# Performance work log

Measured on AMD Instinct MI355X. Metric: run time of the kernel, lower is better.

The kernel has to match this reference:

```python
import jax, jax.numpy as jnp
import numpy as np
from jax import lax

B, S, H, L, NH, DH, FF, C, V, P = 8, 512, 768, 12, 12, 64, 3072, 9, 30522, 512
INV_SQRT_DH = 1.0 / float(np.sqrt(DH))

def _ln(x, s, b, eps=1e-12):
    m = x.mean(-1, keepdims=True)
    v = x.var(-1, keepdims=True)
    return (x - m) / jnp.sqrt(v + eps) * s + b

def _encode(input_ids, attention_mask, fl):
    (tok_emb, pos_emb, type_emb, emb_ln_s, emb_ln_b, qkv_w, qkv_b, ao_w, ao_b,
     ln1_s, ln1_b, ff1_w, ff1_b, ff2_w, ff2_b, ln2_s, ln2_b, head_w, head_b,
     trans, start_t, end_t) = fl
    x = tok_emb[input_ids] + pos_emb[None, :S] + type_emb[0]   # token_type_ids=None -> all zeros
    x = _ln(x, emb_ln_s, emb_ln_b)
    bias = (1.0 - attention_mask.astype(x.dtype))[:, None, None, :] * -1e4
    for i in range(L):
        qkv = x @ qkv_w[i] + qkv_b[i]
        q, k, v = [t.reshape(B, S, NH, DH).transpose(0, 2, 1, 3) for t in jnp.split(qkv, 3, axis=-1)]
        a = jax.nn.softmax(jnp.einsum('bhqd,bhkd->bhqk', q, k) * INV_SQRT_DH + bias, axis=-1)
        ctx = jnp.einsum('bhqk,bhkd->bhqd', a, v).transpose(0, 2, 1, 3).reshape(B, S, H)
        x = _ln(x + ctx @ ao_w[i] + ao_b[i], ln1_s[i], ln1_b[i])
        hmid = jax.nn.gelu(x @ ff1_w[i] + ff1_b[i], approximate=False)
        x = _ln(x + hmid @ ff2_w[i] + ff2_b[i], ln2_s[i], ln2_b[i])
    return x @ head_w + head_b  # emissions [B,S,C]; dropout is identity in eval

def _crf_llh(em, tags, mask, trans, start_t, end_t):
    # pytorch-crf: sum over batch of (numerator - log partition)
    b = jnp.arange(em.shape[0])
    mf = mask.astype(em.dtype)
    num = start_t[tags[:, 0]] + em[b, 0, tags[:, 0]]
    tr = trans[tags[:, :-1], tags[:, 1:]]                                    # [B,S-1]
    es = jnp.take_along_axis(em[:, 1:], tags[:, 1:, None], axis=2)[..., 0]   # [B,S-1]
    num = num + jnp.sum((tr + es) * mf[:, 1:], axis=1)
    last = (mask.sum(1) - 1).astype(jnp.int32)
    num = num + end_t[jnp.take_along_axis(tags, last[:, None], 1)[:, 0]]
    def step(alpha, xs):
        e_t, m_t = xs  # [B,C], [B]
        nxt = jax.scipy.special.logsumexp(alpha[:, :, None] + trans[None] + e_t[:, None, :], axis=1)
        return jnp.where(m_t[:, None], nxt, alpha), None
    alpha0 = start_t + em[:, 0]
    alpha, _ = lax.scan(step, alpha0, (em[:, 1:].transpose(1, 0, 2), mask[:, 1:].T))
    logZ = jax.scipy.special.logsumexp(alpha + end_t, axis=1)
    return jnp.sum(num - logZ)

def _viterbi(em, mask, trans, start_t, end_t):
    def step(score, xs):
        e_t, m_t = xs
        cand = score[:, :, None] + trans[None]   # [B,C,C]
        idx = jnp.argmax(cand, axis=1)           # [B,C] backpointers
        best = jnp.max(cand, axis=1) + e_t
        return jnp.where(m_t[:, None], best, score), idx
    score, hist = lax.scan(step, start_t + em[:, 0], (em[:, 1:].transpose(1, 0, 2), mask[:, 1:].T))
    last = jnp.argmax(score + end_t, axis=1)     # [B]
    def back(tag, xs):
        idx_t, m_t = xs
        prev = jnp.take_along_axis(idx_t, tag[:, None], 1)[:, 0]
        return jnp.where(m_t, prev, tag), tag
    first, rest = lax.scan(back, last, (hist, mask[:, 1:].T), reverse=True)
    return jnp.concatenate([first[:, None], rest.T], axis=1)  # [B,S]

def setup_inputs():
    key = jax.random.key(0)
    ks = iter(jax.random.split(key, 32))
    p = lambda shape, s=0.02: (jax.random.normal(next(ks), shape) * s).astype(jnp.float32)
    return dict(
        input_ids=jax.random.randint(next(ks), (B, S), 0, V),
        attention_mask=jnp.ones((B, S), dtype=jnp.int32),
        labels=jax.random.randint(next(ks), (B, S), 0, C),
        tok_emb=p((V, H)), pos_emb=p((P, H)), type_emb=p((2, H)),
        emb_ln_s=jnp.ones((H,), jnp.float32), emb_ln_b=jnp.zeros((H,), jnp.float32),
        qkv_w=p((L, H, 3 * H)), qkv_b=jnp.zeros((L, 3 * H), jnp.float32),
        ao_w=p((L, H, H)), ao_b=jnp.zeros((L, H), jnp.float32),
        ln1_s=jnp.ones((L, H), jnp.float32), ln1_b=jnp.zeros((L, H), jnp.float32),
        ff1_w=p((L, H, FF)), ff1_b=jnp.zeros((L, FF), jnp.float32),
        ff2_w=p((L, FF, H)), ff2_b=jnp.zeros((L, H), jnp.float32),
        ln2_s=jnp.ones((L, H), jnp.float32), ln2_b=jnp.zeros((L, H), jnp.float32),
        head_w=p((H, C)), head_b=jnp.zeros((C,), jnp.float32),
        trans=p((C, C), 0.1), start_t=p((C,), 0.1), end_t=p((C,), 0.1),
    )

def reference(input_ids, attention_mask, labels, tok_emb, pos_emb, type_emb, emb_ln_s, emb_ln_b,
              qkv_w, qkv_b, ao_w, ao_b, ln1_s, ln1_b, ff1_w, ff1_b, ff2_w, ff2_b, ln2_s, ln2_b,
              head_w, head_b, trans, start_t, end_t):
    fl = (tok_emb, pos_emb, type_emb, emb_ln_s, emb_ln_b, qkv_w, qkv_b, ao_w, ao_b,
          ln1_s, ln1_b, ff1_w, ff1_b, ff2_w, ff2_b, ln2_s, ln2_b, head_w, head_b,
          trans, start_t, end_t)
    em = _encode(input_ids, attention_mask, fl)
    mask = attention_mask.astype(bool)
    neg_llh = -_crf_llh(em, labels, mask, trans, start_t, end_t)
    tags = _viterbi(em, mask, trans, start_t, end_t)
    return (neg_llh, tags)
```

## Files before the change

### kernel.cpp

```cpp
#include <hip/hip_runtime.h>
#include <hip/hip_bf16.h>
#include <math.h>

#define HDIM 768
#define SEQ 512
#define BATCH 8
#define NHEAD 12
#define DHEAD 64
#define FFDIM 3072
#define NLAYER 12
#define NCLS 9

typedef _Float16 half8 __attribute__((ext_vector_type(8)));
typedef _Float16 half4v __attribute__((ext_vector_type(4)));
typedef float f32x4 __attribute__((ext_vector_type(4)));

#define OFF_QKV 0
#define OFF_AO  (768*2304)
#define OFF_FF1 (768*2304 + 768*768)
#define OFF_FF2 (768*2304 + 768*768 + 768*3072)
#define WELEMS  (768*2304 + 768*768 + 768*3072 + 3072*768)

__device__ __forceinline__ float block_sum_256(float v, float* red) {
  #pragma unroll
  for (int o = 32; o > 0; o >>= 1) v += __shfl_down(v, o);
  int t = threadIdx.x;
  if ((t & 63) == 0) red[t >> 6] = v;
  __syncthreads();
  float r = red[0] + red[1] + red[2] + red[3];
  __syncthreads();
  return r;
}

__global__ __launch_bounds__(256) void embed_ln_kernel(
    const int* __restrict__ ids, const float* __restrict__ tok,
    const float* __restrict__ pos, const float* __restrict__ typ,
    const float* __restrict__ gamma, const float* __restrict__ beta,
    float* __restrict__ xout)
{
  __shared__ float red[4];
  int row = blockIdx.x;
  int t = threadIdx.x;
  int s = row & (SEQ - 1);
  int id = ids[row];
  float v[3];
  #pragma unroll
  for (int k = 0; k < 3; k++) {
    int d = t + k * 256;
    v[k] = tok[(size_t)id * HDIM + d] + pos[(size_t)s * HDIM + d] + typ[d];
  }
  float total = block_sum_256(v[0] + v[1] + v[2], red);
  float mean = total * (1.0f / 768.0f);
  float sq = 0.0f;
  #pragma unroll
  for (int k = 0; k < 3; k++) { float d = v[k] - mean; sq += d * d; }
  float var = block_sum_256(sq, red) * (1.0f / 768.0f);
  float inv = rsqrtf(var + 1e-12f);
  #pragma unroll
  for (int k = 0; k < 3; k++) {
    int d = t + k * 256;
    xout[(size_t)row * HDIM + d] = (v[k] - mean) * inv * gamma[d] + beta[d];
  }
}

__global__ __launch_bounds__(256) void ln_kernel(
    const float* __restrict__ in, const float* __restrict__ gamma,
    const float* __restrict__ beta, float* __restrict__ outp)
{
  __shared__ float red[4];
  int row = blockIdx.x, t = threadIdx.x;
  const float* ip = in + (size_t)row * HDIM;
  float v[3];
  #pragma unroll
  for (int k = 0; k < 3; k++) v[k] = ip[t + k * 256];
  float total = block_sum_256(v[0] + v[1] + v[2], red);
  float mean = total * (1.0f / 768.0f);
  float sq = 0.0f;
  #pragma unroll
  for (int k = 0; k < 3; k++) { float d = v[k] - mean; sq += d * d; }
  float var = block_sum_256(sq, red) * (1.0f / 768.0f);
  float inv = rsqrtf(var + 1e-12f);
  float* op = outp + (size_t)row * HDIM;
  #pragma unroll
  for (int k = 0; k < 3; k++) {
    int d = t + k * 256;
    op[d] = (v[k] - mean) * inv * gamma[d] + beta[d];
  }
}

__global__ __launch_bounds__(256) void convert_w_kernel(
    const float* __restrict__ w_qkv, const float* __restrict__ w_ao,
    const float* __restrict__ w_ff1, const float* __restrict__ w_ff2,
    _Float16* __restrict__ hi, _Float16* __restrict__ lo)
{
  int bid = blockIdx.x;
  const float* src; int K, N; size_t off; int tb;
  if (bid < 432)       { src = w_qkv; K = 768;  N = 2304; off = OFF_QKV; tb = bid; }
  else if (bid < 576)  { src = w_ao;  K = 768;  N = 768;  off = OFF_AO;  tb = bid - 432; }
  else if (bid < 1152) { src = w_ff1; K = 768;  N = 3072; off = OFF_FF1; tb = bid - 576; }
  else                 { src = w_ff2; K = 3072; N = 768;  off = OFF_FF2; tb = bid - 1152; }
  int ntn = N >> 6;
  int k0 = (tb / ntn) * 64, n0 = (tb % ntn) * 64;
  __shared__ float tile[64][65];
  int t = threadIdx.x;
  int r = t >> 4, c4 = (t & 15) * 4;
  #pragma unroll
  for (int i = 0; i < 4; i++) {
    float4 v = *(const float4*)(src + (size_t)(k0 + r + 16 * i) * N + n0 + c4);
    tile[r + 16 * i][c4 + 0] = v.x;
    tile[r + 16 * i][c4 + 1] = v.y;
    tile[r + 16 * i][c4 + 2] = v.z;
    tile[r + 16 * i][c4 + 3] = v.w;
  }
  __syncthreads();
  #pragma unroll
  for (int o = 0; o < 4; o++) {
    int n = r + 16 * o;
    half4v hv, lv;
    #pragma unroll
    for (int j = 0; j < 4; j++) {
      float x = tile[c4 + j][n];
      _Float16 h = (_Float16)x;
      hv[j] = h;
      lv[j] = (_Float16)(x - (float)h);
    }
    size_t idx = off + (size_t)(n0 + n) * K + k0 + c4;
    *(half4v*)&hi[idx] = hv;
    *(half4v*)&lo[idx] = lv;
  }
}

__device__ __forceinline__ float gelu_exact(float x) {
  return 0.5f * x * (1.0f + erff(x * 0.70710678118654752440f));
}

template<int BM, bool GELU, bool RES>
__global__ __launch_bounds__(256) void gemm_mfma(
    const float* __restrict__ A, const _Float16* __restrict__ WTh,
    const _Float16* __restrict__ WTl, const float* __restrict__ bias,
    const float* __restrict__ Rsrc, float* __restrict__ C,
    int M, int N, int K)
{
  constexpr int MI = BM / 32;
  constexpr int TPR = 256 / BM;
  constexpr int AW = BM / 8;
  __shared__ _Float16 Ah[BM][40], Al[BM][40];
  __shared__ _Float16 Bh[128][40], Bl[128][40];

  int t = threadIdx.x;
  int n0 = blockIdx.x * 128, m0 = blockIdx.y * BM;
  int wave = t >> 6, lane = t & 63;
  int wm = (wave >> 1) * (BM / 2), wn = (wave & 1) * 64;
  int r15 = lane & 15, kg = lane >> 4;

  int ar = t / TPR, ac = (t % TPR) * AW;
  int br = t >> 1, bc = (t & 1) * 16;
  const float* Ap = A + (size_t)(m0 + ar) * K + ac;
  const _Float16* Bph = WTh + (size_t)(n0 + br) * K + bc;
  const _Float16* Bpl = WTl + (size_t)(n0 + br) * K + bc;

  f32x4 acc[MI][4];
  #pragma unroll
  for (int i = 0; i < MI; i++)
    #pragma unroll
    for (int j = 0; j < 4; j++) acc[i][j] = (f32x4){0.f, 0.f, 0.f, 0.f};

  for (int k0 = 0; k0 < K; k0 += 32) {
    float af[AW];
    #pragma unroll
    for (int c = 0; c < AW / 4; c++) {
      float4 v = *(const float4*)(Ap + k0 + c * 4);
      af[c * 4 + 0] = v.x; af[c * 4 + 1] = v.y;
      af[c * 4 + 2] = v.z; af[c * 4 + 3] = v.w;
    }
    float4 bh0 = *(const float4*)(Bph + k0);
    float4 bh1 = *(const float4*)(Bph + k0 + 8);
    float4 bl0 = *(const float4*)(Bpl + k0);
    float4 bl1 = *(const float4*)(Bpl + k0 + 8);

    __syncthreads();
    #pragma unroll
    for (int c = 0; c < AW / 8; c++) {
      half8 hv, lv;
      #pragma unroll
      for (int e = 0; e < 8; e++) {
        float x = af[c * 8 + e];
        _Float16 h = (_Float16)x;
        hv[e] = h;
        lv[e] = (_Float16)(x - (float)h);
      }
      *(half8*)&Ah[ar][ac + c * 8] = hv;
      *(half8*)&Al[ar][ac + c * 8] = lv;
    }
    *(float4*)&Bh[br][bc]     = bh0;
    *(float4*)&Bh[br][bc + 8] = bh1;
    *(float4*)&Bl[br][bc]     = bl0;
    *(float4*)&Bl[br][bc + 8] = bl1;
    __syncthreads();

    half8 ahf[MI], alf[MI];
    #pragma unroll
    for (int i = 0; i < MI; i++) {
      ahf[i] = *(const half8*)&Ah[wm + i * 16 + r15][kg * 8];
      alf[i] = *(const half8*)&Al[wm + i * 16 + r15][kg * 8];
    }
    #pragma unroll
    for (int j = 0; j < 4; j++) {
      half8 bhf = *(const half8*)&Bh[wn + j * 16 + r15][kg * 8];
      half8 blf = *(const half8*)&Bl[wn + j * 16 + r15][kg * 8];
      #pragma unroll
      for (int i = 0; i < MI; i++) {
        acc[i][j] = __builtin_amdgcn_mfma_f32_16x16x32_f16(ahf[i], bhf, acc[i][j], 0, 0, 0);
        acc[i][j] = __builtin_amdgcn_mfma_f32_16x16x32_f16(ahf[i], blf, acc[i][j], 0, 0, 0);
        acc[i][j] = __builtin_amdgcn_mfma_f32_16x16x32_f16(alf[i], bhf, acc[i][j], 0, 0, 0);
      }
    }
  }

  #pragma unroll
  for (int i = 0; i < MI; i++)
    #pragma unroll
    for (int j = 0; j < 4; j++)
      #pragma unroll
      for (int q = 0; q < 4; q++) {
        int row = m0 + wm + i * 16 + kg * 4 + q;
        int col = n0 + wn + j * 16 + r15;
        float v = acc[i][j][q] + bias[col];
        if (RES) v += Rsrc[(size_t)row * N + col];
        if (GELU) v = gelu_exact(v);
        C[(size_t)row * N + col] = v;
      }
}

__device__ __forceinline__ int swz(int jl, int d) {
  return jl * 64 + ((((d) >> 3) ^ (jl & 7)) << 3) + ((d) & 7);
}

__global__ __launch_bounds__(256) void attn_kernel(
    const float* __restrict__ qkv, const int* __restrict__ maskp,
    float* __restrict__ ctxo)
{
  __shared__ float ss[16][516];
  __shared__ float qs[16][68];
  __shared__ float ks[64 * 64];

  int t = threadIdx.x;
  int qt = blockIdx.x, bh = blockIdx.y;
  int b = bh / NHEAD, h = bh % NHEAD;
  int q0 = qt * 16;
  const float* Qb = qkv + (size_t)b * SEQ * 2304 + h * 64;
  const float* Kb = Qb + 768;
  const float* Vb = Qb + 1536;

  {
    int r = t >> 4, d0 = (t & 15) * 4;
    *(float4*)&qs[r][d0] = *(const float4*)(Qb + (size_t)(q0 + r) * 2304 + d0);
  }
  __syncthreads();

  int r = t >> 4, j16 = t & 15;

  for (int jt = 0; jt < 8; jt++) {
    int kr = t >> 2, kc0 = (t & 3) * 16;
    const float* src = Kb + (size_t)(jt * 64 + kr) * 2304 + kc0;
    float4 kv0 = *(const float4*)(src + 0);
    float4 kv1 = *(const float4*)(src + 4);
    float4 kv2 = *(const float4*)(src + 8);
    float4 kv3 = *(const float4*)(src + 12);
    __syncthreads();
    *(float4*)&ks[swz(kr, kc0 + 0)]  = kv0;
    *(float4*)&ks[swz(kr, kc0 + 4)]  = kv1;
    *(float4*)&ks[swz(kr, kc0 + 8)]  = kv2;
    *(float4*)&ks[swz(kr, kc0 + 12)] = kv3;
    __syncthreads();
    float sacc[4] = {0, 0, 0, 0};
    #pragma unroll
    for (int d0 = 0; d0 < 64; d0 += 4) {
      float4 qv = *(const float4*)&qs[r][d0];
      #pragma unroll
      for (int jj = 0; jj < 4; jj++) {
        int jl = jj * 16 + j16;
        float4 kv = *(const float4*)&ks[swz(jl, d0)];
        sacc[jj] += qv.x * kv.x + qv.y * kv.y + qv.z * kv.z + qv.w * kv.w;
      }
    }
    #pragma unroll
    for (int jj = 0; jj < 4; jj++) {
      int j = jt * 64 + jj * 16 + j16;
      float mb = (1.0f - (float)maskp[b * SEQ + j]) * -10000.0f;
      ss[r][j] = sacc[jj] * 0.125f + mb;
    }
    __syncthreads();
  }

  {
    float mx = -1e30f;
    for (int j = j16; j < 512; j += 16) mx = fmaxf(mx, ss[r][j]);
    #pragma unroll
    for (int o = 1; o < 16; o <<= 1) mx = fmaxf(mx, __shfl_xor(mx, o));
    float l = 0.0f;
    for (int j = j16; j < 512; j += 16) {
      float p = expf(ss[r][j] - mx);
      ss[r][j] = p;
      l += p;
    }
    #pragma unroll
    for (int o = 1; o < 16; o <<= 1) l += __shfl_xor(l, o);
    float inv = 1.0f / l;
    for (int j = j16; j < 512; j += 16) ss[r][j] *= inv;
  }
  __syncthreads();

  int dl = t & 15;
  float acc[4] = {0, 0, 0, 0};
  for (int jt = 0; jt < 8; jt++) {
    int kr = t >> 2, kc0 = (t & 3) * 16;
    const float* src = Vb + (size_t)(jt * 64 + kr) * 2304 + kc0;
    float4 kv0 = *(const float4*)(src + 0);
    float4 kv1 = *(const float4*)(src + 4);
    float4 kv2 = *(const float4*)(src + 8);
    float4 kv3 = *(const float4*)(src + 12);
    __syncthreads();
    *(float4*)&ks[swz(kr, kc0 + 0)]  = kv0;
    *(float4*)&ks[swz(kr, kc0 + 4)]  = kv1;
    *(float4*)&ks[swz(kr, kc0 + 8)]  = kv2;
    *(float4*)&ks[swz(kr, kc0 + 12)] = kv3;
    __syncthreads();
    #pragma unroll
    for (int jl4 = 0; jl4 < 16; jl4++) {
      float4 pv = *(const float4*)&ss[r][jt * 64 + jl4 * 4];
      float pl[4] = {pv.x, pv.y, pv.z, pv.w};
      #pragma unroll
      for (int q = 0; q < 4; q++) {
        int jl = jl4 * 4 + q;
        float4 kv = *(const float4*)&ks[swz(jl, dl * 4)];
        acc[0] += pl[q] * kv.x;
        acc[1] += pl[q] * kv.y;
        acc[2] += pl[q] * kv.z;
        acc[3] += pl[q] * kv.w;
      }
    }
    __syncthreads();
  }
  float4 outv = {acc[0], acc[1], acc[2], acc[3]};
  *(float4*)(ctxo + (size_t)(b * SEQ + q0 + r) * HDIM + h * 64 + dl * 4) = outv;
}

__global__ __launch_bounds__(256) void head_kernel(
    const float* __restrict__ x, const float* __restrict__ W,
    const float* __restrict__ bias, float* __restrict__ em)
{
  int wid = threadIdx.x >> 6, lane = threadIdx.x & 63;
  int row = blockIdx.x * 4 + wid;
  const float* xp = x + (size_t)row * HDIM;
  float xv[12];
  #pragma unroll
  for (int k = 0; k < 12; k++) xv[k] = xp[lane + k * 64];
  for (int c = 0; c < NCLS; c++) {
    float p = 0.0f;
    #pragma unroll
    for (int k = 0; k < 12; k++) p += xv[k] * W[(lane + k * 64) * NCLS + c];
    #pragma unroll
    for (int o = 32; o > 0; o >>= 1) p += __shfl_down(p, o);
    if (lane == 0) em[(size_t)row * NCLS + c] = p + bias[c];
  }
}

__global__ __launch_bounds__(512) void crf_kernel(
    const float* __restrict__ em, const int* __restrict__ labels,
    const int* __restrict__ maskp, const float* __restrict__ trans,
    const float* __restrict__ start_t, const float* __restrict__ end_t,
    float* __restrict__ out)
{
  __shared__ float tr_s[81];
  __shared__ float res[8];
  int t = threadIdx.x;
  if (t < 81) tr_s[t] = trans[t];
  __syncthreads();
  int b = t >> 6, lane = t & 63;
  int j = (lane < NCLS) ? lane : 0;

  float alpha = start_t[j] + em[(size_t)(b * SEQ) * NCLS + j];
  for (int step = 1; step < SEQ; step++) {
    int m = maskp[b * SEQ + step];
    float c[9], mx = -1e30f;
    #pragma unroll
    for (int i = 0; i < 9; i++) {
      float ai = __shfl(alpha, i);
      float v = ai + tr_s[i * 9 + j];
      c[i] = v;
      mx = fmaxf(mx, v);
    }
    float s = 0.0f;
    #pragma unroll
    for (int i = 0; i < 9; i++) s += expf(c[i] - mx);
    float nxt = mx + logf(s) + em[(size_t)(b * SEQ + step) * NCLS + j];
    if (m && lane < NCLS) alpha = nxt;
  }
  float val = (lane < NCLS) ? alpha + end_t[lane] : -1e30f;
  float mx = -1e30f;
  #pragma unroll
  for (int i = 0; i < 9; i++) mx = fmaxf(mx, __shfl(val, i));
  float sm = 0.0f;
  #pragma unroll
  for (int i = 0; i < 9; i++) sm += expf(__shfl(val, i) - mx);
  float logZ = mx + logf(sm);

  float part = 0.0f;
  int cnt = 0;
  for (int step = lane; step < SEQ; step += 64) cnt += maskp[b * SEQ + step];
  for (int step = 1 + lane; step < SEQ; step += 64) {
    if (maskp[b * SEQ + step]) {
      int tp = labels[b * SEQ + step - 1];
      int tc = labels[b * SEQ + step];
      part += tr_s[tp * 9 + tc] + em[(size_t)(b * SEQ + step) * NCLS + tc];
    }
  }
  #pragma unroll
  for (int o = 32; o > 0; o >>= 1) {
    part += __shfl_down(part, o);
    cnt  += __shfl_down(cnt, o);
  }
  if (lane == 0) {
    int t0 = labels[b * SEQ];
    float num = part + start_t[t0] + em[(size_t)(b * SEQ) * NCLS + t0];
    int last = cnt - 1;
    int tl = labels[b * SEQ + last];
    num += end_t[tl];
    res[b] = num - logZ;
  }
  __syncthreads();
  if (t == 0) {
    float s = 0.0f;
    #pragma unroll
    for (int bb = 0; bb < 8; bb++) s += res[bb];
    out[0] = -s;
  }
}

__global__ __launch_bounds__(512) void viterbi_kernel(
    const float* __restrict__ em, const int* __restrict__ maskp,
    const float* __restrict__ trans, const float* __restrict__ start_t,
    const float* __restrict__ end_t, float* __restrict__ tags_out)
{
  __shared__ float tr_s[81];
  __shared__ unsigned char hist[BATCH][SEQ - 1][NCLS];
  int t = threadIdx.x;
  if (t < 81) tr_s[t] = trans[t];
  __syncthreads();
  int b = t >> 6, lane = t & 63;
  int j = (lane < NCLS) ? lane : 0;

  float score = start_t[j] + em[(size_t)(b * SEQ) * NCLS + j];
  for (int step = 1; step < SEQ; step++) {
    float best = -1e30f;
    int bi = 0;
    #pragma unroll
    for (int i = 0; i < 9; i++) {
      float v = __shfl(score, i) + tr_s[i * 9 + j];
      if (v > best) { best = v; bi = i; }
    }
    int m = maskp[b * SEQ + step];
    float e = em[(size_t)(b * SEQ + step) * NCLS + j];
    if (lane < NCLS) hist[b][step - 1][j] = (unsigned char)bi;
    if (m && lane < NCLS) score = best + e;
  }
  __syncthreads();

  float val = (lane < NCLS) ? score + end_t[lane] : -1e30f;
  int last = 0;
  float bb = -1e30f;
  #pragma unroll
  for (int i = 0; i < 9; i++) {
    float v = __shfl(val, i);
    if (v > bb) { bb = v; last = i; }
  }
  if (lane == 0) {
    int tag = last;
    for (int k = SEQ - 2; k >= 0; k--) {
      tags_out[b * SEQ + k + 1] = (float)tag;
      if (maskp[b * SEQ + k + 1]) tag = hist[b][k][tag];
    }
    tags_out[b * SEQ] = (float)tag;
  }
}

extern "C" void kernel_launch(void* const* d_in, const int* in_sizes, int n_in,
                              void* d_out, int out_size, void* d_ws, size_t ws_size,
                              hipStream_t stream) {
  const int*   input_ids      = (const int*)d_in[0];
  const int*   attention_mask = (const int*)d_in[1];
  const int*   labels         = (const int*)d_in[2];
  const float* tok_emb  = (const float*)d_in[3];
  const float* pos_emb  = (const float*)d_in[4];
  const float* type_emb = (const float*)d_in[5];
  const float* emb_ln_s = (const float*)d_in[6];
  const float* emb_ln_b = (const float*)d_in[7];
  const float* qkv_w    = (const float*)d_in[8];
  const float* qkv_b    = (const float*)d_in[9];
  const float* ao_w     = (const float*)d_in[10];
  const float* ao_b     = (const float*)d_in[11];
  const float* ln1_s    = (const float*)d_in[12];
  const float* ln1_b    = (const float*)d_in[13];
  const float* ff1_w    = (const float*)d_in[14];
  const float* ff1_b    = (const float*)d_in[15];
  const float* ff2_w    = (const float*)d_in[16];
  const float* ff2_b    = (const float*)d_in[17];
  const float* ln2_s    = (const float*)d_in[18];
  const float* ln2_b    = (const float*)d_in[19];
  const float* head_w   = (const float*)d_in[20];
  const float* head_b   = (const float*)d_in[21];
  const float* trans    = (const float*)d_in[22];
  const float* start_t  = (const float*)d_in[23];
  const float* end_t    = (const float*)d_in[24];

  const size_t ROWS = (size_t)BATCH * SEQ;
  float* ws   = (float*)d_ws;
  float* x    = ws;
  float* qkvb = x + ROWS * HDIM;
  float* ctxb = qkvb + ROWS * 2304;
  float* hmid = qkvb;
  float* tmp  = ctxb + ROWS * HDIM;
  float* em   = tmp + ROWS * HDIM;
  _Float16* wt_hi = (_Float16*)(em + ROWS * NCLS + 64);
  _Float16* wt_lo = wt_hi + WELEMS;

  embed_ln_kernel<<<ROWS, 256, 0, stream>>>(input_ids, tok_emb, pos_emb,
                                            type_emb, emb_ln_s, emb_ln_b, x);

  for (int i = 0; i < NLAYER; i++) {
    convert_w_kernel<<<1728, 256, 0, stream>>>(
        qkv_w + (size_t)i * HDIM * 2304, ao_w + (size_t)i * HDIM * HDIM,
        ff1_w + (size_t)i * HDIM * FFDIM, ff2_w + (size_t)i * FFDIM * HDIM,
        wt_hi, wt_lo);
    gemm_mfma<128, false, false><<<dim3(18, 32), 256, 0, stream>>>(
        x, wt_hi + OFF_QKV, wt_lo + OFF_QKV, qkv_b + (size_t)i * 2304,
        nullptr, qkvb, 4096, 2304, 768);
    attn_kernel<<<dim3(32, 96), 256, 0, stream>>>(qkvb, attention_mask, ctxb);
    gemm_mfma<64, false, true><<<dim3(6, 64), 256, 0, stream>>>(
        ctxb, wt_hi + OFF_AO, wt_lo + OFF_AO, ao_b + (size_t)i * HDIM,
        x, tmp, 4096, 768, 768);
    ln_kernel<<<ROWS, 256, 0, stream>>>(tmp, ln1_s + (size_t)i * HDIM,
                                        ln1_b + (size_t)i * HDIM, x);
    gemm_mfma<128, true, false><<<dim3(24, 32), 256, 0, stream>>>(
        x, wt_hi + OFF_FF1, wt_lo + OFF_FF1, ff1_b + (size_t)i * FFDIM,
        nullptr, hmid, 4096, 3072, 768);
    gemm_mfma<64, false, true><<<dim3(6, 64), 256, 0, stream>>>(
        hmid, wt_hi + OFF_FF2, wt_lo + OFF_FF2, ff2_b + (size_t)i * HDIM,
        x, tmp, 4096, 768, 3072);
    ln_kernel<<<ROWS, 256, 0, stream>>>(tmp, ln2_s + (size_t)i * HDIM,
                                        ln2_b + (size_t)i * HDIM, x);
  }

  head_kernel<<<1024, 256, 0, stream>>>(x, head_w, head_b, em);
  crf_kernel<<<1, 512, 0, stream>>>(em, labels, attention_mask, trans,
                                    start_t, end_t, (float*)d_out);
  viterbi_kernel<<<1, 512, 0, stream>>>(em, attention_mask, trans, start_t,
                                        end_t, (float*)d_out + 1);
}
```

Before: 7.820 ms.

## Double-buffer GEMM LDS tiles, narrow N tile, and parallelize CRF/Viterbi across blocks

The GEMM now uses two LDS buffers so the next K-tile's global loads are issued while the current tile is computed, with one barrier per iteration instead of two. A BN template parameter gives the output-projection and FF2 GEMMs 64x64 tiles, doubling their grid for better CU occupancy. The CRF log-likelihood and Viterbi decode, previously two single-block kernels run one after the other, are merged into one 8-block kernel that stages emissions and mask in LDS, plus a small finalize kernel. The cost is doubled LDS use per GEMM block and an extra tiny launch.

```diff
diff --git a/kernel.cpp b/kernel.cpp
--- a/kernel.cpp
+++ b/kernel.cpp
@@ -134,80 +134,88 @@
   return 0.5f * x * (1.0f + erff(x * 0.70710678118654752440f));
 }
 
-template<int BM, bool GELU, bool RES>
+template<int BM, int BN, bool GELU, bool RES>
 __global__ __launch_bounds__(256) void gemm_mfma(
     const float* __restrict__ A, const _Float16* __restrict__ WTh,
     const _Float16* __restrict__ WTl, const float* __restrict__ bias,
     const float* __restrict__ Rsrc, float* __restrict__ C,
     int M, int N, int K)
 {
-  constexpr int MI = BM / 32;
-  constexpr int TPR = 256 / BM;
+  constexpr int MI = BM / 32, NJ = BN / 32;
   constexpr int AW = BM / 8;
-  __shared__ _Float16 Ah[BM][40], Al[BM][40];
-  __shared__ _Float16 Bh[128][40], Bl[128][40];
+  constexpr int ATPR = 32 / AW;
+  constexpr int BW = BN / 8;
+  constexpr int BTPR = 32 / BW;
+  __shared__ _Float16 Ah[2][BM][40], Al[2][BM][40];
+  __shared__ _Float16 Bh[2][BN][40], Bl[2][BN][40];
 
   int t = threadIdx.x;
-  int n0 = blockIdx.x * 128, m0 = blockIdx.y * BM;
+  int n0 = blockIdx.x * BN, m0 = blockIdx.y * BM;
   int wave = t >> 6, lane = t & 63;
-  int wm = (wave >> 1) * (BM / 2), wn = (wave & 1) * 64;
+  int wm = (wave >> 1) * (BM / 2), wn = (wave & 1) * (BN / 2);
   int r15 = lane & 15, kg = lane >> 4;
 
-  int ar = t / TPR, ac = (t % TPR) * AW;
-  int br = t >> 1, bc = (t & 1) * 16;
+  int ar = t / ATPR, ac = (t % ATPR) * AW;
+  int br = t / BTPR, bc = (t % BTPR) * BW;
   const float* Ap = A + (size_t)(m0 + ar) * K + ac;
   const _Float16* Bph = WTh + (size_t)(n0 + br) * K + bc;
   const _Float16* Bpl = WTl + (size_t)(n0 + br) * K + bc;
 
-  f32x4 acc[MI][4];
-  #pragma unroll
-  for (int i = 0; i < MI; i++)
-    #pragma unroll
-    for (int j = 0; j < 4; j++) acc[i][j] = (f32x4){0.f, 0.f, 0.f, 0.f};
-
-  for (int k0 = 0; k0 < K; k0 += 32) {
-    float af[AW];
+  float aReg[AW];
+  float4 bhReg[BW / 8], blReg[BW / 8];
+
+  auto load_tile = [&](int kt) {
+    int k0 = kt * 32;
     #pragma unroll
     for (int c = 0; c < AW / 4; c++) {
       float4 v = *(const float4*)(Ap + k0 + c * 4);
-      af[c * 4 + 0] = v.x; af[c * 4 + 1] = v.y;
-      af[c * 4 + 2] = v.z; af[c * 4 + 3] = v.w;
-    }
-    float4 bh0 = *(const float4*)(Bph + k0);
-    float4 bh1 = *(const float4*)(Bph + k0 + 8);
-    float4 bl0 = *(const float4*)(Bpl + k0);
-    float4 bl1 = *(const float4*)(Bpl + k0 + 8);
-
-    __syncthreads();
+      aReg[c * 4 + 0] = v.x; aReg[c * 4 + 1] = v.y;
+      aReg[c * 4 + 2] = v.z; aReg[c * 4 + 3] = v.w;
+    }
+    #pragma unroll
+    for (int c = 0; c < BW / 8; c++) {
+      bhReg[c] = *(const float4*)(Bph + k0 + c * 8);
+      blReg[c] = *(const float4*)(Bpl + k0 + c * 8);
+    }
+  };
+  auto store_lds = [&](int buf) {
     #pragma unroll
     for (int c = 0; c < AW / 8; c++) {
       half8 hv, lv;
       #pragma unroll
       for (int e = 0; e < 8; e++) {
-        float x = af[c * 8 + e];
+        float x = aReg[c * 8 + e];
         _Float16 h = (_Float16)x;
         hv[e] = h;
         lv[e] = (_Float16)(x - (float)h);
       }
-      *(half8*)&Ah[ar][ac + c * 8] = hv;
-      *(half8*)&Al[ar][ac + c * 8] = lv;
-    }
-    *(float4*)&Bh[br][bc]     = bh0;
-    *(float4*)&Bh[br][bc + 8] = bh1;
-    *(float4*)&Bl[br][bc]     = bl0;
-    *(float4*)&Bl[br][bc + 8] = bl1;
-    __syncthreads();
-
+      *(half8*)&Ah[buf][ar][ac + c * 8] = hv;
+      *(half8*)&Al[buf][ar][ac + c * 8] = lv;
+    }
+    #pragma unroll
+    for (int c = 0; c < BW / 8; c++) {
+      *(float4*)&Bh[buf][br][bc + c * 8] = bhReg[c];
+      *(float4*)&Bl[buf][br][bc + c * 8] = blReg[c];
+    }
+  };
+
+  f32x4 acc[MI][NJ];
+  #pragma unroll
+  for (int i = 0; i < MI; i++)
+    #pragma unroll
+    for (int j = 0; j < NJ; j++) acc[i][j] = (f32x4){0.f, 0.f, 0.f, 0.f};
+
+  auto compute = [&](int buf) {
     half8 ahf[MI], alf[MI];
     #pragma unroll
     for (int i = 0; i < MI; i++) {
-      ahf[i] = *(const half8*)&Ah[wm + i * 16 + r15][kg * 8];
-      alf[i] = *(const half8*)&Al[wm + i * 16 + r15][kg * 8];
-    }
-    #pragma unroll
-    for (int j = 0; j < 4; j++) {
-      half8 bhf = *(const half8*)&Bh[wn + j * 16 + r15][kg * 8];
-      half8 blf = *(const half8*)&Bl[wn + j * 16 + r15][kg * 8];
+      ahf[i] = *(const half8*)&Ah[buf][wm + i * 16 + r15][kg * 8];
+      alf[i] = *(const half8*)&Al[buf][wm + i * 16 + r15][kg * 8];
+    }
+    #pragma unroll
+    for (int j = 0; j < NJ; j++) {
+      half8 bhf = *(const half8*)&Bh[buf][wn + j * 16 + r15][kg * 8];
+      half8 blf = *(const half8*)&Bl[buf][wn + j * 16 + r15][kg * 8];
       #pragma unroll
       for (int i = 0; i < MI; i++) {
         acc[i][j] = __builtin_amdgcn_mfma_f32_16x16x32_f16(ahf[i], bhf, acc[i][j], 0, 0, 0);
@@ -215,12 +223,26 @@
         acc[i][j] = __builtin_amdgcn_mfma_f32_16x16x32_f16(alf[i], bhf, acc[i][j], 0, 0, 0);
       }
     }
-  }
+  };
+
+  int NT = K / 32;
+  load_tile(0);
+  store_lds(0);
+  __syncthreads();
+  int cur = 0;
+  for (int kt = 1; kt < NT; kt++) {
+    load_tile(kt);
+    compute(cur);
+    store_lds(cur ^ 1);
+    __syncthreads();
+    cur ^= 1;
+  }
+  compute(cur);
 
   #pragma unroll
   for (int i = 0; i < MI; i++)
     #pragma unroll
-    for (int j = 0; j < 4; j++)
+    for (int j = 0; j < NJ; j++)
       #pragma unroll
       for (int q = 0; q < 4; q++) {
         int row = m0 + wm + i * 16 + kg * 4 + q;
@@ -366,123 +388,128 @@
   }
 }
 
-__global__ __launch_bounds__(512) void crf_kernel(
+__global__ __launch_bounds__(128) void crf_vit_kernel(
     const float* __restrict__ em, const int* __restrict__ labels,
     const int* __restrict__ maskp, const float* __restrict__ trans,
     const float* __restrict__ start_t, const float* __restrict__ end_t,
-    float* __restrict__ out)
-{
+    float* __restrict__ partial, float* __restrict__ tags_out)
+{
+  __shared__ float ems[2][SEQ * NCLS];
+  __shared__ int   msk[2][SEQ];
   __shared__ float tr_s[81];
-  __shared__ float res[8];
+  __shared__ unsigned char hist[2][SEQ - 1][NCLS];
+  __shared__ float res2[2];
+
   int t = threadIdx.x;
-  if (t < 81) tr_s[t] = trans[t];
-  __syncthreads();
-  int b = t >> 6, lane = t & 63;
+  int role = blockIdx.x >> 2;
+  int pair = blockIdx.x & 3;
+  int b0 = pair * 2;
+
+  {
+    const float4* src = (const float4*)(em + (size_t)b0 * SEQ * NCLS);
+    float4* dst = (float4*)&ems[0][0];
+    for (int i = t; i < SEQ * NCLS * 2 / 4; i += 128) dst[i] = src[i];
+    const int4* ms = (const int4*)(maskp + b0 * SEQ);
+    int4* md = (int4*)&msk[0][0];
+    for (int i = t; i < SEQ * 2 / 4; i += 128) md[i] = ms[i];
+    if (t < 81) tr_s[t] = trans[t];
+  }
+  __syncthreads();
+
+  int w = t >> 6, lane = t & 63;
+  int b = b0 + w;
   int j = (lane < NCLS) ? lane : 0;
-
-  float alpha = start_t[j] + em[(size_t)(b * SEQ) * NCLS + j];
-  for (int step = 1; step < SEQ; step++) {
-    int m = maskp[b * SEQ + step];
-    float c[9], mx = -1e30f;
+  const float* E = ems[w];
+  const int* M = msk[w];
+
+  if (role == 0) {
+    float alpha = start_t[j] + E[j];
+    for (int step = 1; step < SEQ; step++) {
+      int m = M[step];
+      float c[9], mx = -1e30f;
+      #pragma unroll
+      for (int i = 0; i < 9; i++) {
+        float v = __shfl(alpha, i) + tr_s[i * 9 + j];
+        c[i] = v;
+        mx = fmaxf(mx, v);
+      }
+      float s = 0.0f;
+      #pragma unroll
+      for (int i = 0; i < 9; i++) s += expf(c[i] - mx);
+      float nxt = mx + logf(s) + E[step * 9 + j];
+      if (m && lane < NCLS) alpha = nxt;
+    }
+    float val = (lane < NCLS) ? alpha + end_t[lane] : -1e30f;
+    float mx = -1e30f;
+    #pragma unroll
+    for (int i = 0; i < 9; i++) mx = fmaxf(mx, __shfl(val, i));
+    float sm = 0.0f;
+    #pragma unroll
+    for (int i = 0; i < 9; i++) sm += expf(__shfl(val, i) - mx);
+    float logZ = mx + logf(sm);
+
+    float part = 0.0f;
+    int cnt = 0;
+    for (int step = lane; step < SEQ; step += 64) cnt += M[step];
+    for (int step = 1 + lane; step < SEQ; step += 64) {
+      if (M[step]) {
+        int tp = labels[b * SEQ + step - 1];
+        int tc = labels[b * SEQ + step];
+        part += tr_s[tp * 9 + tc] + E[step * 9 + tc];
+      }
+    }
+    #pragma unroll
+    for (int o = 32; o > 0; o >>= 1) {
+      part += __shfl_down(part, o);
+      cnt  += __shfl_down(cnt, o);
+    }
+    if (lane == 0) {
+      int t0 = labels[b * SEQ];
+      float num = part + start_t[t0] + E[t0];
+      int last = cnt - 1;
+      int tl = labels[b * SEQ + last];
+      num += end_t[tl];
+      res2[w] = num - logZ;
+    }
+    __syncthreads();
+    if (t == 0) partial[pair] = res2[0] + res2[1];
+  } else {
+    float score = start_t[j] + E[j];
+    for (int step = 1; step < SEQ; step++) {
+      float best = -1e30f;
+      int bi = 0;
+      #pragma unroll
+      for (int i = 0; i < 9; i++) {
+        float v = __shfl(score, i) + tr_s[i * 9 + j];
+        if (v > best) { best = v; bi = i; }
+      }
+      int m = M[step];
+      float e = E[step * 9 + j];
+      if (lane < NCLS) hist[w][step - 1][j] = (unsigned char)bi;
+      if (m && lane < NCLS) score = best + e;
+    }
+    float val = (lane < NCLS) ? score + end_t[lane] : -1e30f;
+    int last = 0;
+    float bb = -1e30f;
     #pragma unroll
     for (int i = 0; i < 9; i++) {
-      float ai = __shfl(alpha, i);
-      float v = ai + tr_s[i * 9 + j];
-      c[i] = v;
-      mx = fmaxf(mx, v);
-    }
-    float s = 0.0f;
-    #pragma unroll
-    for (int i = 0; i < 9; i++) s += expf(c[i] - mx);
-    float nxt = mx + logf(s) + em[(size_t)(b * SEQ + step) * NCLS + j];
-    if (m && lane < NCLS) alpha = nxt;
-  }
-  float val = (lane < NCLS) ? alpha + end_t[lane] : -1e30f;
-  float mx = -1e30f;
-  #pragma unroll
-  for (int i = 0; i < 9; i++) mx = fmaxf(mx, __shfl(val, i));
-  float sm = 0.0f;
-  #pragma unroll
-  for (int i = 0; i < 9; i++) sm += expf(__shfl(val, i) - mx);
-  float logZ = mx + logf(sm);
-
-  float part = 0.0f;
-  int cnt = 0;
-  for (int step = lane; step < SEQ; step += 64) cnt += maskp[b * SEQ + step];
-  for (int step = 1 + lane; step < SEQ; step += 64) {
-    if (maskp[b * SEQ + step]) {
-      int tp = labels[b * SEQ + step - 1];
-      int tc = labels[b * SEQ + step];
-      part += tr_s[tp * 9 + tc] + em[(size_t)(b * SEQ + step) * NCLS + tc];
-    }
-  }
-  #pragma unroll
-  for (int o = 32; o > 0; o >>= 1) {
-    part += __shfl_down(part, o);
-    cnt  += __shfl_down(cnt, o);
-  }
-  if (lane == 0) {
-    int t0 = labels[b * SEQ];
-    float num = part + start_t[t0] + em[(size_t)(b * SEQ) * NCLS + t0];
-    int last = cnt - 1;
-    int tl = labels[b * SEQ + last];
-    num += end_t[tl];
-    res[b] = num - logZ;
-  }
-  __syncthreads();
-  if (t == 0) {
-    float s = 0.0f;
-    #pragma unroll
-    for (int bb = 0; bb < 8; bb++) s += res[bb];
-    out[0] = -s;
-  }
-}
-
-__global__ __launch_bounds__(512) void viterbi_kernel(
-    const float* __restrict__ em, const int* __restrict__ maskp,
-    const float* __restrict__ trans, const float* __restrict__ start_t,
-    const float* __restrict__ end_t, float* __restrict__ tags_out)
-{
-  __shared__ float tr_s[81];
-  __shared__ unsigned char hist[BATCH][SEQ - 1][NCLS];
-  int t = threadIdx.x;
-  if (t < 81) tr_s[t] = trans[t];
-  __syncthreads();
-  int b = t >> 6, lane = t & 63;
-  int j = (lane < NCLS) ? lane : 0;
-
-  float score = start_t[j] + em[(size_t)(b * SEQ) * NCLS + j];
-  for (int step = 1; step < SEQ; step++) {
-    float best = -1e30f;
-    int bi = 0;
-    #pragma unroll
-    for (int i = 0; i < 9; i++) {
-      float v = __shfl(score, i) + tr_s[i * 9 + j];
-      if (v > best) { best = v; bi = i; }
-    }
-    int m = maskp[b * SEQ + step];
-    float e = em[(size_t)(b * SEQ + step) * NCLS + j];
-    if (lane < NCLS) hist[b][step - 1][j] = (unsigned char)bi;
-    if (m && lane < NCLS) score = best + e;
-  }
-  __syncthreads();
-
-  float val = (lane < NCLS) ? score + end_t[lane] : -1e30f;
-  int last = 0;
-  float bb = -1e30f;
-  #pragma unroll
-  for (int i = 0; i < 9; i++) {
-    float v = __shfl(val, i);
-    if (v > bb) { bb = v; last = i; }
-  }
-  if (lane == 0) {
-    int tag = last;
-    for (int k = SEQ - 2; k >= 0; k--) {
-      tags_out[b * SEQ + k + 1] = (float)tag;
-      if (maskp[b * SEQ + k + 1]) tag = hist[b][k][tag];
-    }
-    tags_out[b * SEQ] = (float)tag;
-  }
+      float v = __shfl(val, i);
+      if (v > bb) { bb = v; last = i; }
+    }
+    if (lane == 0) {
+      int tag = last;
+      for (int k = SEQ - 2; k >= 0; k--) {
+        tags_out[b * SEQ + k + 1] = (float)tag;
+        if (M[k + 1]) tag = hist[w][k][tag];
+      }
+      tags_out[b * SEQ] = (float)tag;
+    }
+  }
+}
+
+__global__ void fin_kernel(const float* __restrict__ partial, float* __restrict__ out) {
+  if (threadIdx.x == 0)
+    out[0] = -(partial[0] + partial[1] + partial[2] + partial[3]);
 }
 
 extern "C" void kernel_launch(void* const* d_in, const int* in_sizes, int n_in,
@@ -524,6 +551,7 @@
   float* em   = tmp + ROWS * HDIM;
   _Float16* wt_hi = (_Float16*)(em + ROWS * NCLS + 64);
   _Float16* wt_lo = wt_hi + WELEMS;
+  float* partial = (float*)(wt_lo + WELEMS);
 
   embed_ln_kernel<<<ROWS, 256, 0, stream>>>(input_ids, tok_emb, pos_emb,
                                             type_emb, emb_ln_s, emb_ln_b, x);
@@ -533,19 +561,19 @@
         qkv_w + (size_t)i * HDIM * 2304, ao_w + (size_t)i * HDIM * HDIM,
         ff1_w + (size_t)i * HDIM * FFDIM, ff2_w + (size_t)i * FFDIM * HDIM,
         wt_hi, wt_lo);
-    gemm_mfma<128, false, false><<<dim3(18, 32), 256, 0, stream>>>(
+    gemm_mfma<128, 128, false, false><<<dim3(18, 32), 256, 0, stream>>>(
         x, wt_hi + OFF_QKV, wt_lo + OFF_QKV, qkv_b + (size_t)i * 2304,
         nullptr, qkvb, 4096, 2304, 768);
     attn_kernel<<<dim3(32, 96), 256, 0, stream>>>(qkvb, attention_mask, ctxb);
-    gemm_mfma<64, false, true><<<dim3(6, 64), 256, 0, stream>>>(
+    gemm_mfma<64, 64, false, true><<<dim3(12, 64), 256, 0, stream>>>(
         ctxb, wt_hi + OFF_AO, wt_lo + OFF_AO, ao_b + (size_t)i * HDIM,
         x, tmp, 4096, 768, 768);
     ln_kernel<<<ROWS, 256, 0, stream>>>(tmp, ln1_s + (size_t)i * HDIM,
                                         ln1_b + (size_t)i * HDIM, x);
-    gemm_mfma<128, true, false><<<dim3(24, 32), 256, 0, stream>>>(
+    gemm_mfma<128, 128, true, false><<<dim3(24, 32), 256, 0, stream>>>(
         x, wt_hi + OFF_FF1, wt_lo + OFF_FF1, ff1_b + (size_t)i * FFDIM,
         nullptr, hmid, 4096, 3072, 768);
-    gemm_mfma<64, false, true><<<dim3(6, 64), 256, 0, stream>>>(
+    gemm_mfma<64, 64, false, true><<<dim3(12, 64), 256, 0, stream>>>(
         hmid, wt_hi + OFF_FF2, wt_lo + OFF_FF2, ff2_b + (size_t)i * HDIM,
         x, tmp, 4096, 768, 3072);
     ln_kernel<<<ROWS, 256, 0, stream>>>(tmp, ln2_s + (size_t)i * HDIM,
@@ -553,8 +581,7 @@
   }
 
   head_kernel<<<1024, 256, 0, stream>>>(x, head_w, head_b, em);
-  crf_kernel<<<1, 512, 0, stream>>>(em, labels, attention_mask, trans,
-                                    start_t, end_t, (float*)d_out);
-  viterbi_kernel<<<1, 512, 0, stream>>>(em, attention_mask, trans, start_t,
-                                        end_t, (float*)d_out + 1);
-}
+  crf_vit_kernel<<<8, 128, 0, stream>>>(em, labels, attention_mask, trans,
+                                        start_t, end_t, partial, (float*)d_out + 1);
+  fin_kernel<<<1, 64, 0, stream>>>(partial, (float*)d_out);
+}
```

Result: slower. 8.281 ms (+5.9%).
